# Optimization experiments

Measured on AMD Instinct MI355X. Metric: run time of the kernel, lower is better.

## Reference

```python
import jax, jax.numpy as jnp
import numpy as np

EPS = 1e-8

def squash(s, axis=-1):
    sq = jnp.sum(s * s, axis=axis, keepdims=True)
    return sq / (1.0 + sq) * s / (jnp.sqrt(sq) + EPS)

def setup_inputs() -> dict:
    key = jax.random.key(0)
    k1, k2 = jax.random.split(key)
    B, in_caps, in_dim = 256, 1152, 8
    num_caps, dim_caps = 10, 16
    x = jax.random.normal(k1, (B, in_caps, in_dim), dtype=jnp.float32)
    W = 0.01 * jax.random.normal(k2, (num_caps, in_caps, dim_caps, in_dim), dtype=jnp.float32)
    return {"x": x, "W": W}

def reference(x, W, num_routing=3):
    # u_hat: [B, num_caps, in_caps, dim_caps]
    u_hat = jnp.einsum('ncdi,bci->bncd', W, x)
    u_hat_det = jax.lax.stop_gradient(u_hat)
    B, N, C, D = u_hat.shape
    b = jnp.zeros((B, N, C, 1), dtype=u_hat.dtype)
    for _ in range(num_routing - 1):
        c = jax.nn.softmax(b, axis=1)                 # over num_caps
        s = jnp.sum(c * u_hat_det, axis=2)            # [B, N, D]
        v = squash(s)
        uv = jnp.einsum('bncd,bnd->bnc', u_hat_det, v)[..., None]
        b = b + uv
    c = jax.nn.softmax(b, axis=1)
    s = jnp.sum(c * u_hat, axis=2)
    v = squash(s)                                     # [B, N, D]
    return v
```

## Files before the change

kernel.cpp:

```cpp
#include <hip/hip_runtime.h>
#include <math.h>
#include <stdint.h>

#define B_N 256
#define C_N 1152
#define I_N 8
#define N_N 10
#define D_N 16

constexpr int C_PER    = 18;
constexpr int C_CHUNKS = C_N / C_PER;
constexpr int STAGE_C  = 3;
constexpr int N_STAGES = 6;
constexpr int BLOCK    = 256;

typedef short v8s __attribute__((ext_vector_type(8)));
typedef float v4f __attribute__((ext_vector_type(4)));

constexpr int POOL_BYTES = 32432;

constexpr size_t VSTG_FL = 16 * 16 * 164;
constexpr size_t PS_FL   = (size_t)C_CHUNKS * B_N * 160;
constexpr size_t WB_SH   = (size_t)C_N * 1280;
constexpr size_t XT_SH   = (size_t)1024 * 2304;

#define GLD16(g, l)                                                         \
    __builtin_amdgcn_global_load_lds(                                       \
        (const uint32_t __attribute__((address_space(1)))*)(g),             \
        (uint32_t __attribute__((address_space(3)))*)(l), 16, 0, 0)

__device__ __forceinline__ uint32_t cvtpk(float a, float b) {
    uint32_t r;
    asm("v_cvt_pk_bf16_f32 %0, %1, %2" : "=v"(r) : "v"(a), "v"(b));
    return r;
}
__device__ __forceinline__ float bf2f(short s) {
    return __uint_as_float(((uint32_t)(uint16_t)s) << 16);
}

__global__ __launch_bounds__(BLOCK)
void conv_all(const float* __restrict__ x, const float* __restrict__ W,
              short* __restrict__ Wb, short* __restrict__ xt)
{
    if (blockIdx.x < 144) {
        const int c0 = blockIdx.x * 8;
        const int cc = threadIdx.x >> 5;
        const int k4 = threadIdx.x & 31;
        const float4* W4 = (const float4*)W;
        uint2* dst = (uint2*)Wb;
        for (int n = 0; n < N_N; ++n) {
            float4 v = W4[(size_t)n * 36864 + (size_t)(c0 + cc) * 32 + k4];
            dst[(((size_t)(c0 + cc) * 1280 + n * 128) >> 2) + k4] =
                make_uint2(cvtpk(v.x, v.y), cvtpk(v.z, v.w));
        }
    } else {
        const int tile  = blockIdx.x - 144;
        const int chunk = tile >> 4;
        const int btile = tile & 15;
        const int c0    = chunk * C_PER;
        const int gb0   = btile * 16;
        const float4* x4 = (const float4*)x;
        uint2* dst = (uint2*)(xt + (size_t)tile * 2304);
        #pragma unroll
        for (int it = 0; it < 3; ++it) {
            int f = threadIdx.x + BLOCK * it;
            if (f < 576) {
                int b = f / 36, r = f - b * 36;
                float4 v = x4[(size_t)(gb0 + b) * 2304 + c0 * 2 + r];
                int cp = r >> 1, i0 = (r & 1) * 4;
                dst[((cp * 128 + b * 8 + i0) >> 2)] =
                    make_uint2(cvtpk(v.x, v.y), cvtpk(v.z, v.w));
            }
        }
    }
}

template <bool FIRST>
__global__ __launch_bounds__(BLOCK, 4)
void route_pass(const short* __restrict__ Wb, const short* __restrict__ xt,
                const float* __restrict__ vstG, float* __restrict__ p_s)
{
    __shared__ __align__(16) char pool[POOL_BYTES];
    short* wbuf = (short*)pool;
    short* xs   = (short*)(pool + 15360);
    float* vst  = (float*)(pool + 19968);
    float* cfl  = (float*)(pool + 30464);
    float* comb = (float*)pool;

    const int tid   = threadIdx.x;
    const int wv    = tid >> 6;
    const int lane  = tid & 63;
    const int b     = lane & 15;
    const int quad  = lane >> 4;
    const int chunk = blockIdx.x;
    const int btile = blockIdx.y;
    const int gb0   = btile * 16;
    const int c0    = chunk * C_PER;

    {
        const char* src = (const char*)(xt + (size_t)(chunk * 16 + btile) * 2304);
        #pragma unroll
        for (int it = 0; it < 2; ++it) {
            int f = tid + BLOCK * it;
            if (f < 288) GLD16(src + f * 16, (char*)xs + f * 16);
        }
    }
    asm volatile("" ::: "memory");
    if (!FIRST) {
        const char* src = (const char*)(vstG + (size_t)btile * 2624);
        #pragma unroll
        for (int it = 0; it < 3; ++it) {
            int f = tid + BLOCK * it;
            if (f < 656) GLD16(src + f * 16, (char*)vst + f * 16);
        }
    }
    asm volatile("" ::: "memory");
    #pragma unroll
    for (int s0 = 0; s0 < 2; ++s0) {
        const char* src = (const char*)(Wb + (size_t)(c0 + s0 * STAGE_C) * 1280);
        char* dst = (char*)(wbuf + s0 * (STAGE_C * 1280));
        #pragma unroll
        for (int it = 0; it < 2; ++it) {
            int f = tid + BLOCK * it;
            if (f < 480) GLD16(src + f * 16, dst + f * 16);
        }
        asm volatile("" ::: "memory");
    }
    asm volatile("s_waitcnt vmcnt(2)" ::: "memory");
    __builtin_amdgcn_s_barrier();

    const int ncnt = (wv < 2) ? 3 : 2;
    v4f sacc[3];
    sacc[0] = (v4f){0.f, 0.f, 0.f, 0.f};
    sacc[1] = (v4f){0.f, 0.f, 0.f, 0.f};
    sacc[2] = (v4f){0.f, 0.f, 0.f, 0.f};

    for (int st = 0; st < N_STAGES; ++st) {
        const short* Ws = wbuf + (st & 1) * (STAGE_C * 1280);

        if (st >= 1 && st < N_STAGES - 1) {
            const char* src =
                (const char*)(Wb + (size_t)(c0 + (st + 1) * STAGE_C) * 1280);
            char* dst = (char*)(wbuf + ((st + 1) & 1) * (STAGE_C * 1280));
            #pragma unroll
            for (int it = 0; it < 2; ++it) {
                int f = tid + BLOCK * it;
                if (f < 480) GLD16(src + f * 16, dst + f * 16);
            }
            asm volatile("" ::: "memory");
        }

        if (!FIRST) {
            #pragma unroll
            for (int k = 0; k < 8; ++k) {
                const int idx = wv + 4 * k;
                if (idx < 30) {
                    const int c = idx / 10;
                    const int n = idx - c * 10;
                    v8s wa = {0, 0, 0, 0, 0, 0, 0, 0};
                    if (quad == 0)
                        wa = *(const v8s*)(Ws + c * 1280 + n * 128 + b * 8);
                    const v8s xb =
                        *(const v8s*)(xs + (st * STAGE_C + c) * 128 + b * 8);
                    v4f u = __builtin_amdgcn_mfma_f32_16x16x32_bf16(
                        wa, xb, (v4f){0.f, 0.f, 0.f, 0.f}, 0, 0, 0);
                    const float4 v4 =
                        *(const float4*)(vst + b * 164 + n * 16 + quad * 4);
                    float l = u[0] * v4.x + u[1] * v4.y + u[2] * v4.z + u[3] * v4.w;
                    l += __shfl_xor(l, 16);
                    l += __shfl_xor(l, 32);
                    const float e1 = __expf(l);
                    if (quad == 0) cfl[c * 163 + n * 16 + b] = e1;
                }
            }
            asm volatile("s_waitcnt lgkmcnt(0)" ::: "memory");
            __builtin_amdgcn_s_barrier();
        }

        {
            const bool valid = (quad < STAGE_C);
            const int  cl    = valid ? quad : 0;
            const v8s xq =
                *(const v8s*)(xs + (st * STAGE_C + cl) * 128 + b * 8);
            float xf[8];
            #pragma unroll
            for (int j = 0; j < 8; ++j) xf[j] = bf2f(xq[j]);

            if (FIRST) {
                union { v8s s; uint32_t u[4]; } zu;
                zu.u[0] = cvtpk(0.1f * xf[0], 0.1f * xf[1]);
                zu.u[1] = cvtpk(0.1f * xf[2], 0.1f * xf[3]);
                zu.u[2] = cvtpk(0.1f * xf[4], 0.1f * xf[5]);
                zu.u[3] = cvtpk(0.1f * xf[6], 0.1f * xf[7]);
                #pragma unroll
                for (int jj = 0; jj < 3; ++jj) {
                    if (jj < ncnt) {
                        const int n = wv + 4 * jj;
                        v8s wa = {0, 0, 0, 0, 0, 0, 0, 0};
                        if (valid)
                            wa = *(const v8s*)(Ws + cl * 1280 + n * 128 + b * 8);
                        sacc[jj] = __builtin_amdgcn_mfma_f32_16x16x32_bf16(
                            wa, zu.s, sacc[jj], 0, 0, 0);
                    }
                }
            } else {
                float Z = 0.f;
                #pragma unroll
                for (int n = 0; n < N_N; ++n) Z += cfl[cl * 163 + n * 16 + b];
                const float rzv = __builtin_amdgcn_rcpf(Z);
                #pragma unroll
                for (int jj = 0; jj < 3; ++jj) {
                    if (jj < ncnt) {
                        const int n = wv + 4 * jj;
                        const float cv = cfl[cl * 163 + n * 16 + b] * rzv;
                        union { v8s s; uint32_t u[4]; } zu;
                        zu.u[0] = cvtpk(cv * xf[0], cv * xf[1]);
                        zu.u[1] = cvtpk(cv * xf[2], cv * xf[3]);
                        zu.u[2] = cvtpk(cv * xf[4], cv * xf[5]);
                        zu.u[3] = cvtpk(cv * xf[6], cv * xf[7]);
                        v8s wa = {0, 0, 0, 0, 0, 0, 0, 0};
                        if (valid)
                            wa = *(const v8s*)(Ws + cl * 1280 + n * 128 + b * 8);
                        sacc[jj] = __builtin_amdgcn_mfma_f32_16x16x32_bf16(
                            wa, zu.s, sacc[jj], 0, 0, 0);
                    }
                }
            }
        }

        asm volatile("s_waitcnt vmcnt(0) lgkmcnt(0)" ::: "memory");
        __builtin_amdgcn_s_barrier();
    }

    #pragma unroll
    for (int jj = 0; jj < 3; ++jj) {
        if (jj < ncnt) {
            const int n = wv + 4 * jj;
            #pragma unroll
            for (int r = 0; r < 4; ++r)
                comb[b * 164 + n * 16 + quad * 4 + r] = sacc[jj][r];
        }
    }
    __syncthreads();
    #pragma unroll
    for (int it = 0; it < 3; ++it) {
        int f = tid + BLOCK * it;
        if (f < 640) {
            int e = f * 4;
            int bb = e / 160, rem = e - bb * 160;
            float4 v = *(const float4*)(comb + bb * 164 + rem);
            *(float4*)(&p_s[((size_t)chunk * B_N + gb0 + bb) * 160 + rem]) = v;
        }
    }
}

__global__ __launch_bounds__(BLOCK)
void reduce_squash(const float* __restrict__ p_s, float* __restrict__ vstG,
                   float* __restrict__ out, int phase)
{
    const int warp = threadIdx.x >> 6;
    const int lane = threadIdx.x & 63;
    const int g    = blockIdx.x * 4 + warp;
    const int q    = lane & 3;
    const int h    = lane >> 2;

    float4 s = make_float4(0.f, 0.f, 0.f, 0.f);
    #pragma unroll
    for (int m = 0; m < C_CHUNKS / 16; ++m) {
        const int cc = h + 16 * m;
        float4 v = *(const float4*)(&p_s[((size_t)cc * (B_N * N_N) + g) * D_N + q * 4]);
        s.x += v.x; s.y += v.y; s.z += v.z; s.w += v.w;
    }
    #pragma unroll
    for (int off = 4; off < 64; off <<= 1) {
        s.x += __shfl_xor(s.x, off);
        s.y += __shfl_xor(s.y, off);
        s.z += __shfl_xor(s.z, off);
        s.w += __shfl_xor(s.w, off);
    }
    float sq = s.x * s.x + s.y * s.y + s.z * s.z + s.w * s.w;
    sq += __shfl_xor(sq, 1);
    sq += __shfl_xor(sq, 2);

    const float scale = (sq / (1.f + sq)) / (sqrtf(sq) + 1e-8f);
    const float4 v = make_float4(scale * s.x, scale * s.y, scale * s.z, scale * s.w);

    if (h == 0) {
        if (phase == 2) {
            *(float4*)(&out[(size_t)g * D_N + q * 4]) = v;
        } else {
            const int bb = g / 10, n = g - bb * 10;
            float* vp = vstG + (size_t)(bb >> 4) * 2624 + (bb & 15) * 164 + n * 16 + q * 4;
            if (phase == 0) {
                *(float4*)vp = v;
            } else {
                float4 o = *(const float4*)vp;
                *(float4*)vp = make_float4(o.x + v.x, o.y + v.y, o.z + v.z, o.w + v.w);
            }
        }
    }
}

extern "C" void kernel_launch(void* const* d_in, const int* in_sizes, int n_in,
                              void* d_out, int out_size, void* d_ws, size_t ws_size,
                              hipStream_t stream)
{
    const float* x = (const float*)d_in[0];
    const float* W = (const float*)d_in[1];
    float* out  = (float*)d_out;

    float* vstG = (float*)d_ws;
    float* p_s  = vstG + VSTG_FL;
    short* Wb   = (short*)(p_s + PS_FL);
    short* xt   = Wb + WB_SH;

    conv_all<<<dim3(144 + 1024), BLOCK, 0, stream>>>(x, W, Wb, xt);

    dim3 grid(C_CHUNKS, 16);
    dim3 rgrid((B_N * N_N) / 4);

    route_pass<true><<<grid, BLOCK, 0, stream>>>(Wb, xt, vstG, p_s);
    reduce_squash<<<rgrid, BLOCK, 0, stream>>>(p_s, vstG, out, 0);
    route_pass<false><<<grid, BLOCK, 0, stream>>>(Wb, xt, vstG, p_s);
    reduce_squash<<<rgrid, BLOCK, 0, stream>>>(p_s, vstG, out, 1);
    route_pass<false><<<grid, BLOCK, 0, stream>>>(Wb, xt, vstG, p_s);
    reduce_squash<<<rgrid, BLOCK, 0, stream>>>(p_s, vstG, out, 2);
}
```

Baseline: 129.7 us.

## Fuse routing passes and reductions into one persistent kernel with grid barriers

Replaces six separate route/reduce kernel launches with a single persistent kernel that synchronizes the grid using a hierarchical atomic barrier in global memory. The x tile is loaded into LDS once and reused across all three routing passes, and the reductions are spread across the same blocks. This removes launch gaps and repeated xt loads, but relies on all 1024 blocks being co-resident (4 per CU) and adds spin-wait barrier cost.

```diff
diff --git a/kernel.cpp b/kernel.cpp
--- a/kernel.cpp
+++ b/kernel.cpp
@@ -23,6 +23,7 @@
 constexpr size_t PS_FL   = (size_t)C_CHUNKS * B_N * 160;
 constexpr size_t WB_SH   = (size_t)C_N * 1280;
 constexpr size_t XT_SH   = (size_t)1024 * 2304;
+constexpr int    BAR_W   = 576;
 
 #define GLD16(g, l)                                                         \
     __builtin_amdgcn_global_load_lds(                                       \
@@ -40,9 +41,13 @@
 
 __global__ __launch_bounds__(BLOCK)
 void conv_all(const float* __restrict__ x, const float* __restrict__ W,
-              short* __restrict__ Wb, short* __restrict__ xt)
+              short* __restrict__ Wb, short* __restrict__ xt,
+              uint32_t* __restrict__ bar)
 {
     if (blockIdx.x < 144) {
+        if (blockIdx.x == 0) {
+            for (int i = threadIdx.x; i < BAR_W; i += BLOCK) bar[i] = 0u;
+        }
         const int c0 = blockIdx.x * 8;
         const int cc = threadIdx.x >> 5;
         const int k4 = threadIdx.x & 31;
@@ -75,37 +80,50 @@
     }
 }
 
+__device__ __forceinline__ void gbar(uint32_t* bar, int bid, uint32_t expect)
+{
+    asm volatile("s_waitcnt vmcnt(0) lgkmcnt(0)" ::: "memory");
+    __syncthreads();
+    if (threadIdx.x == 0) {
+        __builtin_amdgcn_fence(__ATOMIC_RELEASE, "agent");
+        uint32_t a = __hip_atomic_fetch_add(&bar[(bid & 15) * 32], 1u,
+                                            __ATOMIC_RELAXED,
+                                            __HIP_MEMORY_SCOPE_AGENT);
+        if (a == 63u) {
+            uint32_t t = __hip_atomic_fetch_add(&bar[16 * 32], 1u,
+                                                __ATOMIC_RELAXED,
+                                                __HIP_MEMORY_SCOPE_AGENT);
+            if (t == 15u) {
+                #pragma unroll
+                for (int i = 0; i < 17; ++i)
+                    __hip_atomic_store(&bar[i * 32], 0u, __ATOMIC_RELAXED,
+                                       __HIP_MEMORY_SCOPE_AGENT);
+                __hip_atomic_fetch_add(&bar[17 * 32], 1u, __ATOMIC_RELEASE,
+                                       __HIP_MEMORY_SCOPE_AGENT);
+            }
+        }
+        while (__hip_atomic_load(&bar[17 * 32], __ATOMIC_RELAXED,
+                                 __HIP_MEMORY_SCOPE_AGENT) < expect)
+            __builtin_amdgcn_s_sleep(2);
+        __builtin_amdgcn_fence(__ATOMIC_ACQUIRE, "agent");
+    }
+    __syncthreads();
+}
+
 template <bool FIRST>
-__global__ __launch_bounds__(BLOCK, 4)
-void route_pass(const short* __restrict__ Wb, const short* __restrict__ xt,
-                const float* __restrict__ vstG, float* __restrict__ p_s)
-{
-    __shared__ __align__(16) char pool[POOL_BYTES];
-    short* wbuf = (short*)pool;
-    short* xs   = (short*)(pool + 15360);
-    float* vst  = (float*)(pool + 19968);
-    float* cfl  = (float*)(pool + 30464);
-    float* comb = (float*)pool;
-
-    const int tid   = threadIdx.x;
-    const int wv    = tid >> 6;
-    const int lane  = tid & 63;
-    const int b     = lane & 15;
-    const int quad  = lane >> 4;
-    const int chunk = blockIdx.x;
-    const int btile = blockIdx.y;
-    const int gb0   = btile * 16;
-    const int c0    = chunk * C_PER;
-
-    {
-        const char* src = (const char*)(xt + (size_t)(chunk * 16 + btile) * 2304);
-        #pragma unroll
-        for (int it = 0; it < 2; ++it) {
-            int f = tid + BLOCK * it;
-            if (f < 288) GLD16(src + f * 16, (char*)xs + f * 16);
-        }
-    }
-    asm volatile("" ::: "memory");
+__device__ __forceinline__ void route_core(
+    short* wbuf, const short* xs, float* vst, float* cfl, float* comb,
+    const short* __restrict__ Wb, const float* __restrict__ vstG,
+    float* __restrict__ p_s, int chunk, int btile)
+{
+    const int tid  = threadIdx.x;
+    const int wv   = tid >> 6;
+    const int lane = tid & 63;
+    const int b    = lane & 15;
+    const int quad = lane >> 4;
+    const int gb0  = btile * 16;
+    const int c0   = chunk * C_PER;
+
     if (!FIRST) {
         const char* src = (const char*)(vstG + (size_t)btile * 2624);
         #pragma unroll
@@ -113,8 +131,8 @@
             int f = tid + BLOCK * it;
             if (f < 656) GLD16(src + f * 16, (char*)vst + f * 16);
         }
-    }
-    asm volatile("" ::: "memory");
+        asm volatile("" ::: "memory");
+    }
     #pragma unroll
     for (int s0 = 0; s0 < 2; ++s0) {
         const char* src = (const char*)(Wb + (size_t)(c0 + s0 * STAGE_C) * 1280);
@@ -254,15 +272,17 @@
     }
 }
 
-__global__ __launch_bounds__(BLOCK)
-void reduce_squash(const float* __restrict__ p_s, float* __restrict__ vstG,
-                   float* __restrict__ out, int phase)
-{
-    const int warp = threadIdx.x >> 6;
+__device__ __forceinline__ void reduce_core(const float* __restrict__ p_s,
+                                            float* __restrict__ vstG,
+                                            float* __restrict__ out,
+                                            int phase, int bid)
+{
+    const int wv   = threadIdx.x >> 6;
     const int lane = threadIdx.x & 63;
-    const int g    = blockIdx.x * 4 + warp;
-    const int q    = lane & 3;
-    const int h    = lane >> 2;
+    const int g    = wv * 1024 + bid;
+    if (g >= B_N * N_N) return;
+    const int q = lane & 3;
+    const int h = lane >> 2;
 
     float4 s = make_float4(0.f, 0.f, 0.f, 0.f);
     #pragma unroll
@@ -301,6 +321,47 @@
     }
 }
 
+__global__ __launch_bounds__(BLOCK, 4)
+void fused_route(const short* __restrict__ Wb, const short* __restrict__ xt,
+                 float* __restrict__ vstG, float* __restrict__ p_s,
+                 float* __restrict__ out, uint32_t* bar)
+{
+    __shared__ __align__(16) char pool[POOL_BYTES];
+    short* wbuf = (short*)pool;
+    short* xs   = (short*)(pool + 15360);
+    float* vst  = (float*)(pool + 19968);
+    float* cfl  = (float*)(pool + 30464);
+    float* comb = (float*)pool;
+
+    const int chunk = blockIdx.x;
+    const int btile = blockIdx.y;
+    const int bid   = btile * 64 + chunk;
+    const int tid   = threadIdx.x;
+
+    {
+        const char* src = (const char*)(xt + (size_t)(chunk * 16 + btile) * 2304);
+        #pragma unroll
+        for (int it = 0; it < 2; ++it) {
+            int f = tid + BLOCK * it;
+            if (f < 288) GLD16(src + f * 16, (char*)xs + f * 16);
+        }
+        asm volatile("" ::: "memory");
+    }
+
+    route_core<true>(wbuf, xs, vst, cfl, comb, Wb, vstG, p_s, chunk, btile);
+    gbar(bar, bid, 1);
+    reduce_core(p_s, vstG, out, 0, bid);
+    gbar(bar, bid, 2);
+
+    #pragma unroll 1
+    for (int pass = 1; pass <= 2; ++pass) {
+        route_core<false>(wbuf, xs, vst, cfl, comb, Wb, vstG, p_s, chunk, btile);
+        gbar(bar, bid, (uint32_t)(2 * pass + 1));
+        reduce_core(p_s, vstG, out, pass == 2 ? 2 : 1, bid);
+        if (pass == 1) gbar(bar, bid, 4);
+    }
+}
+
 extern "C" void kernel_launch(void* const* d_in, const int* in_sizes, int n_in,
                               void* d_out, int out_size, void* d_ws, size_t ws_size,
                               hipStream_t stream)
@@ -313,16 +374,8 @@
     float* p_s  = vstG + VSTG_FL;
     short* Wb   = (short*)(p_s + PS_FL);
     short* xt   = Wb + WB_SH;
-
-    conv_all<<<dim3(144 + 1024), BLOCK, 0, stream>>>(x, W, Wb, xt);
-
-    dim3 grid(C_CHUNKS, 16);
-    dim3 rgrid((B_N * N_N) / 4);
-
-    route_pass<true><<<grid, BLOCK, 0, stream>>>(Wb, xt, vstG, p_s);
-    reduce_squash<<<rgrid, BLOCK, 0, stream>>>(p_s, vstG, out, 0);
-    route_pass<false><<<grid, BLOCK, 0, stream>>>(Wb, xt, vstG, p_s);
-    reduce_squash<<<rgrid, BLOCK, 0, stream>>>(p_s, vstG, out, 1);
-    route_pass<false><<<grid, BLOCK, 0, stream>>>(Wb, xt, vstG, p_s);
-    reduce_squash<<<rgrid, BLOCK, 0, stream>>>(p_s, vstG, out, 2);
-}
+    uint32_t* bar = (uint32_t*)(xt + XT_SH);
+
+    conv_all<<<dim3(144 + 1024), BLOCK, 0, stream>>>(x, W, Wb, xt, bar);
+    fused_route<<<dim3(C_CHUNKS, 16), BLOCK, 0, stream>>>(Wb, xt, vstG, p_s, out, bar);
+}
```

After: 252.0 us. 94.3% more time.
